# Kernel optimization log

Hardware: AMD Instinct MI355X
Metric: run time of the kernel (lower is better)

The kernel has to match this reference:

```python
import jax, jax.numpy as jnp
import numpy as np

EMBED_DIM = 768
OUT_DIM = 768
EPS = 1e-06


def setup_inputs() -> dict:
    key = jax.random.key(0)
    ks = jax.random.split(key, 7)
    s_in = 1.0 / np.sqrt(EMBED_DIM)
    x = jax.random.normal(ks[0], (32, 1024, EMBED_DIM), dtype=jnp.float32)
    Wq = jax.random.normal(ks[1], (OUT_DIM, EMBED_DIM), dtype=jnp.float32) * s_in
    bq = jax.random.normal(ks[2], (OUT_DIM,), dtype=jnp.float32) * 0.01
    Wk = jax.random.normal(ks[3], (OUT_DIM, EMBED_DIM), dtype=jnp.float32) * s_in
    bk = jax.random.normal(ks[4], (OUT_DIM,), dtype=jnp.float32) * 0.01
    Wv = jax.random.normal(ks[5], (OUT_DIM, EMBED_DIM), dtype=jnp.float32) * s_in
    bv = jax.random.normal(ks[6], (OUT_DIM,), dtype=jnp.float32) * 0.01
    return {"x": x, "Wq": Wq, "bq": bq, "Wk": Wk, "bk": bk, "Wv": Wv, "bv": bv}


def reference(x, Wq, bq, Wk, bk, Wv, bv):
    # Q/K/V projections: nn.Linear computes x @ W.T + b
    Q = jnp.einsum('bnd,od->bno', x, Wq) + bq  # [B, N, O]
    K = jnp.einsum('bnd,od->bno', x, Wk) + bk
    V = jnp.einsum('bnd,od->bno', x, Wv) + bv
    scale = jnp.sqrt(jnp.asarray(OUT_DIM, dtype=x.dtype)) + EPS
    attn = jnp.einsum('bqo,bko->bqk', Q, K) / scale  # [B, N, N]
    weights = jax.nn.softmax(attn, axis=-1)
    # dropout p=0.0 -> identity (eval/inference)
    return jnp.einsum('bqk,bko->bqo', weights, V)
```

## Files before the change

kernel.cpp:

```cpp
#include <hip/hip_runtime.h>
#include <hip/hip_bf16.h>


typedef float  floatx4  __attribute__((ext_vector_type(4)));
typedef float  floatx16 __attribute__((ext_vector_type(16)));
typedef short  short8   __attribute__((ext_vector_type(8)));

__device__ __forceinline__ unsigned cvtpk(float lo, float hi) {
    unsigned r;
    asm("v_cvt_pk_bf16_f32 %0, %1, %2" : "=v"(r) : "v"(lo), "v"(hi));
    return r;
}
__device__ __forceinline__ floatx16 mfma32(short8 a, short8 b, floatx16 c) {
    return __builtin_amdgcn_mfma_f32_32x32x16_bf16(a, b, c, 0, 0, 0);
}
__device__ __forceinline__ void load_lds16(const void* g, void* lds) {
    __builtin_amdgcn_global_load_lds(
        (const __attribute__((address_space(1))) unsigned int*)g,
        (__attribute__((address_space(3))) unsigned int*)lds, 16, 0, 0);
}
__device__ __forceinline__ void bar_lds() {
    asm volatile("s_waitcnt lgkmcnt(0)" ::: "memory");
    __builtin_amdgcn_s_barrier();
    __builtin_amdgcn_sched_barrier(0);
}
__device__ __forceinline__ void bar_vm() {
    asm volatile("s_waitcnt vmcnt(0)" ::: "memory");
    __builtin_amdgcn_s_barrier();
    __builtin_amdgcn_sched_barrier(0);
}

__global__ __launch_bounds__(256) void cvt_bf16(
    const float* __restrict__ s0, unsigned short* __restrict__ d0, int n0,
    const float* __restrict__ s1, unsigned short* __restrict__ d1, int n1,
    const float* __restrict__ s2, unsigned short* __restrict__ d2, int n2,
    const float* __restrict__ W,  unsigned short* __restrict__ Wf)
{
    if (blockIdx.x >= 2048) {
        const int i = (blockIdx.x - 2048) * 256 + threadIdx.x;
        const int o  = i / 96;
        const int d0i = (i % 96) * 8;
        const floatx4* s = (const floatx4*)(W + (size_t)o * 768 + d0i);
        floatx4 v0 = s[0], v1 = s[1];
        uint4 st;
        st.x = cvtpk(v0[0], v0[1]);
        st.y = cvtpk(v0[2], v0[3]);
        st.z = cvtpk(v1[0], v1[1]);
        st.w = cvtpk(v1[2], v1[3]);
        const size_t idx = (((size_t)(o >> 5) * 48 + (d0i >> 4)) * 64
                            + ((o & 31) | (((d0i >> 3) & 1) << 5))) * 8;
        *reinterpret_cast<uint4*>(Wf + idx) = st;
        return;
    }
    const int stride = 2048 * 256;
    const int base   = blockIdx.x * 256 + threadIdx.x;
    const float* ss[3] = {s0, s1, s2};
    unsigned short* dd[3] = {d0, d1, d2};
    const int nn[3] = {n0, n1, n2};
#pragma unroll
    for (int j = 0; j < 3; ++j) {
        const floatx4* s = (const floatx4*)ss[j];
        uint4* d = (uint4*)dd[j];
        for (int i = base; i < nn[j]; i += stride) {
            floatx4 v0 = s[2 * i];
            floatx4 v1 = s[2 * i + 1];
            uint4 o;
            o.x = cvtpk(v0[0], v0[1]);
            o.y = cvtpk(v0[2], v0[3]);
            o.z = cvtpk(v1[0], v1[1]);
            o.w = cvtpk(v1[2], v1[3]);
            d[i] = o;
        }
    }
}

template <int MODE>
__global__ __launch_bounds__(256, 2) void gemm_lds(
    const unsigned short* __restrict__ A,
    const unsigned short* __restrict__ B,
    unsigned short* __restrict__ C, const float* __restrict__ bias,
    float alpha)
{
    __shared__ __align__(16) unsigned short As[2][128 * 64];
    __shared__ __align__(16) unsigned short Bs[2][128 * 64];

    const int tid = threadIdx.x;
    const int l   = tid & 63;
    const int w   = tid >> 6;
    const int wr  = w >> 1;
    const int wc  = w & 1;
    const int lo5 = l & 31;
    const int hi  = l >> 5;
    const int i0  = blockIdx.x * 128;
    const int j0  = blockIdx.y * 128;

    const int srow = l >> 3;
    const int sc16 = (l & 7) ^ srow;
    const unsigned short* Ag = A + (size_t)(i0 + srow) * 768 + sc16 * 8;
    const unsigned short* Bg = B + (size_t)(j0 + srow) * 768 + sc16 * 8;

    floatx16 acc[2][2] = {};

    auto STAGE = [&](int buf, int kt) {
        const int k0 = kt * 64;
#pragma unroll
        for (int t4 = 0; t4 < 4; ++t4) {
            const int t = w * 4 + t4;
            load_lds16(Ag + (size_t)t * 8 * 768 + k0, &As[buf][t * 512]);
            load_lds16(Bg + (size_t)t * 8 * 768 + k0, &Bs[buf][t * 512]);
        }
    };
    auto COMPUTE = [&](int buf) {
        const char* Ab = (const char*)As[buf];
        const char* Bb = (const char*)Bs[buf];
#pragma unroll
        for (int kk = 0; kk < 4; ++kk) {
            short8 a[2], b[2];
#pragma unroll
            for (int i = 0; i < 2; ++i) {
                const int r = wr * 64 + i * 32 + lo5;
                const unsigned off = r * 128 + ((unsigned)((kk * 2 + hi) ^ (r & 7)) << 4);
                a[i] = *reinterpret_cast<const short8*>(Ab + off);
            }
#pragma unroll
            for (int j = 0; j < 2; ++j) {
                const int r = wc * 64 + j * 32 + lo5;
                const unsigned off = r * 128 + ((unsigned)((kk * 2 + hi) ^ (r & 7)) << 4);
                b[j] = *reinterpret_cast<const short8*>(Bb + off);
            }
#pragma unroll
            for (int i = 0; i < 2; ++i)
#pragma unroll
                for (int j = 0; j < 2; ++j)
                    acc[i][j] = mfma32(a[i], b[j], acc[i][j]);
        }
    };

    STAGE(0, 0);
    __syncthreads();
#pragma unroll 1
    for (int kt = 0; kt < 12; ++kt) {
        if (kt + 1 < 12) STAGE((kt + 1) & 1, kt + 1);
        COMPUTE(kt & 1);
        __syncthreads();
    }

#pragma unroll
    for (int i = 0; i < 2; ++i) {
        float bvv[16];
        if (MODE == 0) {
#pragma unroll
            for (int r = 0; r < 16; ++r) {
                const int ol = (r & 3) + 8 * (r >> 2) + 4 * hi;
                bvv[r] = bias[i0 + wr * 64 + i * 32 + ol];
            }
        }
#pragma unroll
        for (int j = 0; j < 2; ++j) {
            float bj = 0.f;
            if (MODE == 1) bj = bias[j0 + wc * 64 + j * 32 + lo5];
            float v[16];
#pragma unroll
            for (int r = 0; r < 16; ++r)
                v[r] = (MODE == 0) ? (acc[i][j][r] + bvv[r]) * alpha
                                   : (acc[i][j][r] + bj);
#pragma unroll
            for (int cc = 0; cc < 2; ++cc) {
                unsigned w0 = cvtpk(v[8 * cc + 0], v[8 * cc + 1]);
                unsigned w1 = cvtpk(v[8 * cc + 2], v[8 * cc + 3]);
                unsigned w2 = cvtpk(v[8 * cc + 4], v[8 * cc + 5]);
                unsigned w3 = cvtpk(v[8 * cc + 6], v[8 * cc + 7]);
                unsigned x0 = __shfl_xor(w0, 32);
                unsigned x1 = __shfl_xor(w1, 32);
                unsigned x2 = __shfl_xor(w2, 32);
                unsigned x3 = __shfl_xor(w3, 32);
                uint4 st;
                st.x = hi ? x2 : w0;
                st.y = hi ? x3 : w1;
                st.z = hi ? w2 : x0;
                st.w = hi ? w3 : x1;
                size_t idx;
                if (MODE == 0) {
                    const int og = i0 + wr * 64 + i * 32 + cc * 16;
                    const int mg = j0 + wc * 64 + j * 32 + lo5;
                    idx = ((size_t)(mg >> 5) * 48 + (og >> 4)) * 512
                        + (size_t)(lo5 | (hi << 5)) * 8;
                } else {
                    const int ng = i0 + wr * 64 + i * 32 + cc * 16;
                    const int dg = j0 + wc * 64 + j * 32 + lo5;
                    idx = ((size_t)(ng >> 4) * 24 + (dg >> 5)) * 512
                        + (size_t)(lo5 | (hi << 5)) * 8;
                }
                *reinterpret_cast<uint4*>(C + idx) = st;
            }
        }
    }
}

__global__ __launch_bounds__(512, 1) void attn_kernel(
    const unsigned short* __restrict__ Wqf,
    const unsigned short* __restrict__ Kf,
    const unsigned short* __restrict__ Vf,
    const float* __restrict__ x,
    const float* __restrict__ bq,
    float* __restrict__ out)
{
    __shared__ __align__(16) unsigned short Q_lds[96 * 512];
    __shared__ __align__(16) unsigned short P_lds[2][32 * 512];

    const int tid = threadIdx.x;
    const int l   = tid & 63;
    const int w   = tid >> 6;
    const int lo5 = l & 31;
    const int hi  = l >> 5;

    const int bid = blockIdx.x;
    const int xcd = bid & 7;
    const int jj  = bid >> 3;
    const int b   = (jj >> 4) * 8 + xcd;
    const int qi  = jj & 15;
    const int q0  = qi * 64;

    const float MFIX  = 12.0f;
    const float alpha = 1.0f / (sqrtf(768.0f) + 1e-6f);

    const short8* Kp = reinterpret_cast<const short8*>(Kf)
                       + ((size_t)b * 32 * 48) * 64 + l;
    const short8* Vp = reinterpret_cast<const short8*>(Vf)
                       + ((size_t)b * 64 * 24) * 64 + l;

    floatx16 acc6[6] = {};
    short8 kbuf[8], vbuf[4][3];

    {
        float* Xs0 = (float*)P_lds[0];
        float* Xs1 = (float*)P_lds[1];
        const float* xg = x + (size_t)(b * 1024 + q0) * 768;
        const short8* Wp = reinterpret_cast<const short8*>(Wqf) + l;

        const int c16 = tid & 31;
        const int r0  = tid >> 5;

        auto XSTAGE = [&](int p, float* Xs) {
#pragma unroll
            for (int it = 0; it < 4; ++it) {
                const int row = it * 16 + r0;
                const int u   = it * 512 + tid;
                load_lds16(xg + (size_t)row * 768 + p * 128 + ((c16 ^ (row & 7)) << 2),
                           &Xs[u * 4]);
            }
        };

        XSTAGE(0, Xs0);
        bar_vm();

        short8 wbuf2[2][3];
#pragma unroll 1
        for (int p = 0; p < 6; ++p) {
            float* Xs = (p & 1) ? Xs1 : Xs0;
#pragma unroll
            for (int jo = 0; jo < 3; ++jo)
                wbuf2[0][jo] = Wp[(size_t)((w * 3 + jo) * 48 + p * 8) * 64];
            if (p + 1 < 6) XSTAGE(p + 1, (p & 1) ? Xs0 : Xs1);
#pragma unroll
            for (int it = 0; it < 8; ++it) {
                const int ks = p * 8 + it;
                if (it + 1 < 8) {
#pragma unroll
                    for (int jo = 0; jo < 3; ++jo)
                        wbuf2[(it + 1) & 1][jo] =
                            Wp[(size_t)((w * 3 + jo) * 48 + ks + 1) * 64];
                }
                short8 xf[2];
#pragma unroll
                for (int jq = 0; jq < 2; ++jq) {
                    const int row = jq * 32 + lo5;
                    const int un  = it * 4 + hi * 2;
                    floatx4 f0 = *reinterpret_cast<const floatx4*>(
                        &Xs[((row << 5) + ((un + 0) ^ (row & 7))) * 4]);
                    floatx4 f1 = *reinterpret_cast<const floatx4*>(
                        &Xs[((row << 5) + ((un + 1) ^ (row & 7))) * 4]);
                    unsigned q0w = cvtpk(f0[0], f0[1]);
                    unsigned q1w = cvtpk(f0[2], f0[3]);
                    unsigned q2w = cvtpk(f1[0], f1[1]);
                    unsigned q3w = cvtpk(f1[2], f1[3]);
                    uint4 u4 = {q0w, q1w, q2w, q3w};
                    xf[jq] = __builtin_bit_cast(short8, u4);
                }
                __builtin_amdgcn_s_setprio(1);
#pragma unroll
                for (int jo = 0; jo < 3; ++jo) {
#pragma unroll
                    for (int jq = 0; jq < 2; ++jq)
                        acc6[jo * 2 + jq] = mfma32(wbuf2[it & 1][jo], xf[jq],
                                                   acc6[jo * 2 + jq]);
                }
                __builtin_amdgcn_s_setprio(0);
            }
            bar_vm();
        }

        {
            const short8* Kc0 = Kp + (size_t)w * 48 * 64;
#pragma unroll
            for (int u = 0; u < 8; ++u) kbuf[u] = Kc0[(size_t)u * 64];
        }

#pragma unroll
        for (int jo = 0; jo < 3; ++jo) {
            const int o32 = w * 96 + jo * 32;
            float bvv[16];
#pragma unroll
            for (int r = 0; r < 16; ++r)
                bvv[r] = bq[o32 + (r & 3) + 8 * (r >> 2) + 4 * hi];
#pragma unroll
            for (int jq = 0; jq < 2; ++jq) {
                float v[16];
#pragma unroll
                for (int r = 0; r < 16; ++r)
                    v[r] = (acc6[jo * 2 + jq][r] + bvv[r]) * alpha;
#pragma unroll
                for (int cc = 0; cc < 2; ++cc) {
                    unsigned w0 = cvtpk(v[8 * cc + 0], v[8 * cc + 1]);
                    unsigned w1 = cvtpk(v[8 * cc + 2], v[8 * cc + 3]);
                    unsigned w2 = cvtpk(v[8 * cc + 4], v[8 * cc + 5]);
                    unsigned w3 = cvtpk(v[8 * cc + 6], v[8 * cc + 7]);
                    unsigned x0 = __shfl_xor(w0, 32);
                    unsigned x1 = __shfl_xor(w1, 32);
                    unsigned x2 = __shfl_xor(w2, 32);
                    unsigned x3 = __shfl_xor(w3, 32);
                    uint4 st;
                    st.x = hi ? x2 : w0;
                    st.y = hi ? x3 : w1;
                    st.z = hi ? w2 : x0;
                    st.w = hi ? w3 : x1;
                    const int ks_t = w * 6 + jo * 2 + cc;
                    *reinterpret_cast<uint4*>(
                        &Q_lds[((ks_t * 2 + jq) * 64 + (lo5 | (hi << 5))) * 8]) = st;
                }
            }
        }
    }
    bar_lds();

#pragma unroll
    for (int i = 0; i < 6; ++i) acc6[i] = (floatx16){};

    float l_reg0 = 0.f, l_reg1 = 0.f;

#pragma unroll 1
    for (int c = 0; c < 4; ++c) {
        floatx16 s0 = {}, s1 = {};
        const short8* Kc = Kp + (size_t)(c * 8 + w) * 48 * 64;
        short8 qa0 = *reinterpret_cast<const short8*>(&Q_lds[(0 * 64 + l) * 8]);
        short8 qa1 = *reinterpret_cast<const short8*>(&Q_lds[(1 * 64 + l) * 8]);
#pragma unroll 1
        for (int ks8 = 0; ks8 < 6; ++ks8) {
#pragma unroll
            for (int u = 0; u < 8; ++u) {
                const int ks = ks8 * 8 + u;
                short8 ka = kbuf[u];
                if (ks + 8 < 48) kbuf[u] = Kc[(size_t)(ks + 8) * 64];
                short8 qn0, qn1;
                if (ks + 1 < 48) {
                    qn0 = *reinterpret_cast<const short8*>(&Q_lds[(((ks + 1) * 2 + 0) * 64 + l) * 8]);
                    qn1 = *reinterpret_cast<const short8*>(&Q_lds[(((ks + 1) * 2 + 1) * 64 + l) * 8]);
                }
                __builtin_amdgcn_s_setprio(1);
                s0 = mfma32(ka, qa0, s0);
                s1 = mfma32(ka, qa1, s1);
                __builtin_amdgcn_s_setprio(0);
                qa0 = qn0;
                qa1 = qn1;
            }
        }

        const short8* Vc = Vp + (size_t)(c * 16) * 24 * 64;
#pragma unroll
        for (int g = 0; g < 4; ++g)
#pragma unroll
            for (int jv = 0; jv < 3; ++jv)
                vbuf[g][jv] = Vc[((size_t)g * 24 + w * 3 + jv) * 64];

        if (c < 3) {
            const short8* Kn = Kp + (size_t)((c + 1) * 8 + w) * 48 * 64;
#pragma unroll
            for (int u = 0; u < 8; ++u) kbuf[u] = Kn[(size_t)u * 64];
        }

        float p0[16], p1[16];
        float sum0 = 0.f, sum1 = 0.f;
#pragma unroll
        for (int r = 0; r < 16; ++r) {
            p0[r] = __expf(s0[r] - MFIX); sum0 += p0[r];
            p1[r] = __expf(s1[r] - MFIX); sum1 += p1[r];
        }
        l_reg0 += sum0 + __shfl_xor(sum0, 32);
        l_reg1 += sum1 + __shfl_xor(sum1, 32);

        char* Pb = (char*)P_lds[c & 1];
#pragma unroll
        for (int cc = 0; cc < 2; ++cc) {
#pragma unroll
            for (int jt = 0; jt < 2; ++jt) {
                const float* p = jt ? p1 : p0;
                unsigned w0 = cvtpk(p[8 * cc + 0], p[8 * cc + 1]);
                unsigned w1 = cvtpk(p[8 * cc + 2], p[8 * cc + 3]);
                unsigned w2 = cvtpk(p[8 * cc + 4], p[8 * cc + 5]);
                unsigned w3 = cvtpk(p[8 * cc + 6], p[8 * cc + 7]);
                unsigned x0 = __shfl_xor(w0, 32);
                unsigned x1 = __shfl_xor(w1, 32);
                unsigned x2 = __shfl_xor(w2, 32);
                unsigned x3 = __shfl_xor(w3, 32);
                uint4 st;
                st.x = hi ? x2 : w0;
                st.y = hi ? x3 : w1;
                st.z = hi ? w2 : x0;
                st.w = hi ? w3 : x1;
                const unsigned off = (((unsigned)(w * 2 + cc) * 2 + jt) * 64 + l) * 16;
                *reinterpret_cast<uint4*>(Pb + off) = st;
            }
        }
        bar_lds();

        short8 pa0 = *reinterpret_cast<const short8*>(Pb + ((0 * 64 + l) * 16));
        short8 pa1 = *reinterpret_cast<const short8*>(Pb + ((1 * 64 + l) * 16));
#pragma unroll
        for (int g = 0; g < 16; ++g) {
            short8 pn0, pn1;
            if (g + 1 < 16) {
                pn0 = *reinterpret_cast<const short8*>(Pb + ((((g + 1) * 2 + 0) * 64 + l) * 16));
                pn1 = *reinterpret_cast<const short8*>(Pb + ((((g + 1) * 2 + 1) * 64 + l) * 16));
            }
            short8 v0 = vbuf[g & 3][0];
            short8 v1 = vbuf[g & 3][1];
            short8 v2 = vbuf[g & 3][2];
            if (g < 12) {
#pragma unroll
                for (int jv = 0; jv < 3; ++jv)
                    vbuf[g & 3][jv] = Vc[((size_t)(g + 4) * 24 + w * 3 + jv) * 64];
            }
            __builtin_amdgcn_s_setprio(1);
            acc6[0] = mfma32(pa0, v0, acc6[0]);
            acc6[3] = mfma32(pa1, v0, acc6[3]);
            acc6[1] = mfma32(pa0, v1, acc6[1]);
            acc6[4] = mfma32(pa1, v1, acc6[4]);
            acc6[2] = mfma32(pa0, v2, acc6[2]);
            acc6[5] = mfma32(pa1, v2, acc6[5]);
            __builtin_amdgcn_s_setprio(0);
            pa0 = pn0;
            pa1 = pn1;
        }
    }

    bar_lds();
    float* lred = (float*)Q_lds;
    if (hi == 0) {
        lred[(w * 2 + 0) * 32 + lo5] = l_reg0;
        lred[(w * 2 + 1) * 32 + lo5] = l_reg1;
    }
    bar_lds();
    float lt0 = 0.f, lt1 = 0.f;
#pragma unroll
    for (int wv = 0; wv < 8; ++wv) {
        lt0 += lred[(wv * 2 + 0) * 32 + lo5];
        lt1 += lred[(wv * 2 + 1) * 32 + lo5];
    }
    const float li0 = 1.0f / lt0;
    const float li1 = 1.0f / lt1;

#pragma unroll
    for (int jt = 0; jt < 2; ++jt)
#pragma unroll
        for (int r = 0; r < 16; ++r) {
            const int qr = (r & 3) + 8 * (r >> 2) + 4 * hi;
            const float linv = __shfl(jt ? li1 : li0, qr);
            const size_t grow = (size_t)(b * 1024 + q0 + jt * 32 + qr) * 768;
#pragma unroll
            for (int jv = 0; jv < 3; ++jv)
                out[grow + (w * 3 + jv) * 32 + lo5] = acc6[jt * 3 + jv][r] * linv;
        }
}

extern "C" void kernel_launch(void* const* d_in, const int* in_sizes, int n_in,
                              void* d_out, int out_size, void* d_ws, size_t ws_size,
                              hipStream_t stream) {
    const float* x  = (const float*)d_in[0];
    const float* Wq = (const float*)d_in[1];
    const float* bq = (const float*)d_in[2];
    const float* Wk = (const float*)d_in[3];
    const float* bk = (const float*)d_in[4];
    const float* Wv = (const float*)d_in[5];
    const float* bv = (const float*)d_in[6];
    float* out = (float*)d_out;

    unsigned short* Wqf = (unsigned short*)d_ws;
    unsigned short* Kf  = (unsigned short*)d_ws + 25165824u;
    unsigned short* Vf  = (unsigned short*)d_ws + 50331648u;

    unsigned short* xb  = (unsigned short*)d_out;
    unsigned short* Wkb = (unsigned short*)d_out + 25165824u;
    unsigned short* Wvb = Wkb + 589824u;

    cvt_bf16<<<2336, 256, 0, stream>>>(x, xb, 3145728,
                                       Wk, Wkb, 73728,
                                       Wv, Wvb, 73728,
                                       Wq, Wqf);

    gemm_lds<0><<<dim3(6, 256), 256, 0, stream>>>(Wkb, xb, Kf, bk, 1.0f);
    gemm_lds<1><<<dim3(256, 6), 256, 0, stream>>>(xb, Wvb, Vf, bv, 1.0f);

    attn_kernel<<<dim3(512), 512, 0, stream>>>(Wqf, Kf, Vf, x, bq, out);
}
```

Before: 306.1 us.

## Process 512-key chunks with two K tiles per wave, halving barrier rounds

The attention loop now covers 512 keys per outer iteration instead of 256. Each wave computes two 32-key score tiles, so every Q fragment read from LDS feeds four MFMAs instead of two, and the number of softmax/PV rounds and barriers is halved. The P buffer becomes a single larger buffer with a trailing barrier instead of double-buffering. K/V register prefetch depth is shortened, which may expose more global-load latency, while register pressure rises from the extra score accumulators.

```diff
diff --git a/kernel.cpp b/kernel.cpp
--- a/kernel.cpp
+++ b/kernel.cpp
@@ -206,7 +206,7 @@
     float* __restrict__ out)
 {
     __shared__ __align__(16) unsigned short Q_lds[96 * 512];
-    __shared__ __align__(16) unsigned short P_lds[2][32 * 512];
+    __shared__ __align__(16) unsigned short P_lds[64 * 512];
 
     const int tid = threadIdx.x;
     const int l   = tid & 63;
@@ -230,11 +230,11 @@
                        + ((size_t)b * 64 * 24) * 64 + l;
 
     floatx16 acc6[6] = {};
-    short8 kbuf[8], vbuf[4][3];
+    short8 kbA[4], kbB[4], vbuf[2][3];
 
     {
-        float* Xs0 = (float*)P_lds[0];
-        float* Xs1 = (float*)P_lds[1];
+        float* Xs0 = (float*)P_lds;
+        float* Xs1 = (float*)(P_lds + 16 * 512 * 2);
         const float* xg = x + (size_t)(b * 1024 + q0) * 768;
         const short8* Wp = reinterpret_cast<const short8*>(Wqf) + l;
 
@@ -300,10 +300,10 @@
             bar_vm();
         }
 
-        {
-            const short8* Kc0 = Kp + (size_t)w * 48 * 64;
-#pragma unroll
-            for (int u = 0; u < 8; ++u) kbuf[u] = Kc0[(size_t)u * 64];
+#pragma unroll
+        for (int u = 0; u < 4; ++u) {
+            kbA[u] = Kp[((size_t)(0 * 16 + w) * 48 + u) * 64];
+            kbB[u] = Kp[((size_t)(0 * 16 + 8 + w) * 48 + u) * 64];
         }
 
 #pragma unroll
@@ -347,113 +347,118 @@
     for (int i = 0; i < 6; ++i) acc6[i] = (floatx16){};
 
     float l_reg0 = 0.f, l_reg1 = 0.f;
+    char* Pb = (char*)P_lds;
 
 #pragma unroll 1
-    for (int c = 0; c < 4; ++c) {
-        floatx16 s0 = {}, s1 = {};
-        const short8* Kc = Kp + (size_t)(c * 8 + w) * 48 * 64;
-        short8 qa0 = *reinterpret_cast<const short8*>(&Q_lds[(0 * 64 + l) * 8]);
-        short8 qa1 = *reinterpret_cast<const short8*>(&Q_lds[(1 * 64 + l) * 8]);
+    for (int c = 0; c < 2; ++c) {
+        floatx16 sA0 = {}, sA1 = {}, sB0 = {}, sB1 = {};
+        const short8* KcA = Kp + (size_t)(c * 16 + w) * 48 * 64;
+        const short8* KcB = Kp + (size_t)(c * 16 + 8 + w) * 48 * 64;
 #pragma unroll 1
-        for (int ks8 = 0; ks8 < 6; ++ks8) {
-#pragma unroll
-            for (int u = 0; u < 8; ++u) {
-                const int ks = ks8 * 8 + u;
-                short8 ka = kbuf[u];
-                if (ks + 8 < 48) kbuf[u] = Kc[(size_t)(ks + 8) * 64];
-                short8 qn0, qn1;
-                if (ks + 1 < 48) {
-                    qn0 = *reinterpret_cast<const short8*>(&Q_lds[(((ks + 1) * 2 + 0) * 64 + l) * 8]);
-                    qn1 = *reinterpret_cast<const short8*>(&Q_lds[(((ks + 1) * 2 + 1) * 64 + l) * 8]);
-                }
+        for (int k4 = 0; k4 < 12; ++k4) {
+#pragma unroll
+            for (int u = 0; u < 4; ++u) {
+                const int ks = k4 * 4 + u;
+                short8 ka = kbA[u];
+                short8 kb = kbB[u];
+                if (ks + 4 < 48) {
+                    kbA[u] = KcA[(size_t)(ks + 4) * 64];
+                    kbB[u] = KcB[(size_t)(ks + 4) * 64];
+                }
+                short8 qa0 = *reinterpret_cast<const short8*>(&Q_lds[((ks * 2 + 0) * 64 + l) * 8]);
+                short8 qa1 = *reinterpret_cast<const short8*>(&Q_lds[((ks * 2 + 1) * 64 + l) * 8]);
                 __builtin_amdgcn_s_setprio(1);
-                s0 = mfma32(ka, qa0, s0);
-                s1 = mfma32(ka, qa1, s1);
+                sA0 = mfma32(ka, qa0, sA0);
+                sA1 = mfma32(ka, qa1, sA1);
+                sB0 = mfma32(kb, qa0, sB0);
+                sB1 = mfma32(kb, qa1, sB1);
                 __builtin_amdgcn_s_setprio(0);
-                qa0 = qn0;
-                qa1 = qn1;
-            }
-        }
-
-        const short8* Vc = Vp + (size_t)(c * 16) * 24 * 64;
-#pragma unroll
-        for (int g = 0; g < 4; ++g)
+            }
+        }
+
+        const short8* Vc = Vp + (size_t)(c * 32) * 24 * 64;
+#pragma unroll
+        for (int g = 0; g < 2; ++g)
 #pragma unroll
             for (int jv = 0; jv < 3; ++jv)
                 vbuf[g][jv] = Vc[((size_t)g * 24 + w * 3 + jv) * 64];
 
-        if (c < 3) {
-            const short8* Kn = Kp + (size_t)((c + 1) * 8 + w) * 48 * 64;
-#pragma unroll
-            for (int u = 0; u < 8; ++u) kbuf[u] = Kn[(size_t)u * 64];
-        }
-
-        float p0[16], p1[16];
+        float pA0[16], pA1[16], pB0[16], pB1[16];
         float sum0 = 0.f, sum1 = 0.f;
 #pragma unroll
         for (int r = 0; r < 16; ++r) {
-            p0[r] = __expf(s0[r] - MFIX); sum0 += p0[r];
-            p1[r] = __expf(s1[r] - MFIX); sum1 += p1[r];
+            pA0[r] = __expf(sA0[r] - MFIX); sum0 += pA0[r];
+            pA1[r] = __expf(sA1[r] - MFIX); sum1 += pA1[r];
+            pB0[r] = __expf(sB0[r] - MFIX); sum0 += pB0[r];
+            pB1[r] = __expf(sB1[r] - MFIX); sum1 += pB1[r];
         }
         l_reg0 += sum0 + __shfl_xor(sum0, 32);
         l_reg1 += sum1 + __shfl_xor(sum1, 32);
 
-        char* Pb = (char*)P_lds[c & 1];
-#pragma unroll
-        for (int cc = 0; cc < 2; ++cc) {
-#pragma unroll
-            for (int jt = 0; jt < 2; ++jt) {
-                const float* p = jt ? p1 : p0;
-                unsigned w0 = cvtpk(p[8 * cc + 0], p[8 * cc + 1]);
-                unsigned w1 = cvtpk(p[8 * cc + 2], p[8 * cc + 3]);
-                unsigned w2 = cvtpk(p[8 * cc + 4], p[8 * cc + 5]);
-                unsigned w3 = cvtpk(p[8 * cc + 6], p[8 * cc + 7]);
-                unsigned x0 = __shfl_xor(w0, 32);
-                unsigned x1 = __shfl_xor(w1, 32);
-                unsigned x2 = __shfl_xor(w2, 32);
-                unsigned x3 = __shfl_xor(w3, 32);
-                uint4 st;
-                st.x = hi ? x2 : w0;
-                st.y = hi ? x3 : w1;
-                st.z = hi ? w2 : x0;
-                st.w = hi ? w3 : x1;
-                const unsigned off = (((unsigned)(w * 2 + cc) * 2 + jt) * 64 + l) * 16;
-                *reinterpret_cast<uint4*>(Pb + off) = st;
+#pragma unroll
+        for (int S = 0; S < 2; ++S) {
+#pragma unroll
+            for (int cc = 0; cc < 2; ++cc) {
+#pragma unroll
+                for (int jt = 0; jt < 2; ++jt) {
+                    const float* p = S ? (jt ? pB1 : pB0) : (jt ? pA1 : pA0);
+                    unsigned w0 = cvtpk(p[8 * cc + 0], p[8 * cc + 1]);
+                    unsigned w1 = cvtpk(p[8 * cc + 2], p[8 * cc + 3]);
+                    unsigned w2 = cvtpk(p[8 * cc + 4], p[8 * cc + 5]);
+                    unsigned w3 = cvtpk(p[8 * cc + 6], p[8 * cc + 7]);
+                    unsigned x0 = __shfl_xor(w0, 32);
+                    unsigned x1 = __shfl_xor(w1, 32);
+                    unsigned x2 = __shfl_xor(w2, 32);
+                    unsigned x3 = __shfl_xor(w3, 32);
+                    uint4 st;
+                    st.x = hi ? x2 : w0;
+                    st.y = hi ? x3 : w1;
+                    st.z = hi ? w2 : x0;
+                    st.w = hi ? w3 : x1;
+                    const unsigned ku = (unsigned)((S ? 8 + w : w) * 2 + cc);
+                    const unsigned off = ((ku * 2 + jt) * 64 + l) * 16;
+                    *reinterpret_cast<uint4*>(Pb + off) = st;
+                }
+            }
+        }
+
+        if (c == 0) {
+#pragma unroll
+            for (int u = 0; u < 4; ++u) {
+                kbA[u] = Kp[((size_t)(16 + w) * 48 + u) * 64];
+                kbB[u] = Kp[((size_t)(16 + 8 + w) * 48 + u) * 64];
             }
         }
         bar_lds();
 
-        short8 pa0 = *reinterpret_cast<const short8*>(Pb + ((0 * 64 + l) * 16));
-        short8 pa1 = *reinterpret_cast<const short8*>(Pb + ((1 * 64 + l) * 16));
-#pragma unroll
-        for (int g = 0; g < 16; ++g) {
-            short8 pn0, pn1;
-            if (g + 1 < 16) {
-                pn0 = *reinterpret_cast<const short8*>(Pb + ((((g + 1) * 2 + 0) * 64 + l) * 16));
-                pn1 = *reinterpret_cast<const short8*>(Pb + ((((g + 1) * 2 + 1) * 64 + l) * 16));
-            }
-            short8 v0 = vbuf[g & 3][0];
-            short8 v1 = vbuf[g & 3][1];
-            short8 v2 = vbuf[g & 3][2];
-            if (g < 12) {
-#pragma unroll
-                for (int jv = 0; jv < 3; ++jv)
-                    vbuf[g & 3][jv] = Vc[((size_t)(g + 4) * 24 + w * 3 + jv) * 64];
-            }
-            __builtin_amdgcn_s_setprio(1);
-            acc6[0] = mfma32(pa0, v0, acc6[0]);
-            acc6[3] = mfma32(pa1, v0, acc6[3]);
-            acc6[1] = mfma32(pa0, v1, acc6[1]);
-            acc6[4] = mfma32(pa1, v1, acc6[4]);
-            acc6[2] = mfma32(pa0, v2, acc6[2]);
-            acc6[5] = mfma32(pa1, v2, acc6[5]);
-            __builtin_amdgcn_s_setprio(0);
-            pa0 = pn0;
-            pa1 = pn1;
-        }
-    }
-
-    bar_lds();
+#pragma unroll 1
+        for (int g2 = 0; g2 < 16; ++g2) {
+#pragma unroll
+            for (int h = 0; h < 2; ++h) {
+                const int g = g2 * 2 + h;
+                short8 v0 = vbuf[h][0];
+                short8 v1 = vbuf[h][1];
+                short8 v2 = vbuf[h][2];
+                if (g + 2 < 32) {
+#pragma unroll
+                    for (int jv = 0; jv < 3; ++jv)
+                        vbuf[h][jv] = Vc[((size_t)(g + 2) * 24 + w * 3 + jv) * 64];
+                }
+                short8 pa0 = *reinterpret_cast<const short8*>(Pb + (((g * 2 + 0) * 64 + l) * 16));
+                short8 pa1 = *reinterpret_cast<const short8*>(Pb + (((g * 2 + 1) * 64 + l) * 16));
+                __builtin_amdgcn_s_setprio(1);
+                acc6[0] = mfma32(pa0, v0, acc6[0]);
+                acc6[3] = mfma32(pa1, v0, acc6[3]);
+                acc6[1] = mfma32(pa0, v1, acc6[1]);
+                acc6[4] = mfma32(pa1, v1, acc6[4]);
+                acc6[2] = mfma32(pa0, v2, acc6[2]);
+                acc6[5] = mfma32(pa1, v2, acc6[5]);
+                __builtin_amdgcn_s_setprio(0);
+            }
+        }
+        bar_lds();
+    }
+
     float* lred = (float*)Q_lds;
     if (hi == 0) {
         lred[(w * 2 + 0) * 32 + lo5] = l_reg0;
```

New measurement: 321.2 us. 1.05x slower.

## Halve attention query tile to 32 rows for more blocks and occupancy

Applied to the files above, without the earlier changes.

The attention kernel now processes 32 query rows per block instead of 64, doubling the grid to 1024 blocks. LDS buffers and register accumulators are halved and launch bounds request up to 4 blocks per CU, so more waves can be resident to hide latency. In exchange, each block re-reads the full K and V tiles and the Wq slice, so global and L2 traffic per unit of work roughly doubles. MFMA reuse of each K/V fragment also drops from two query tiles to one.

```diff
diff --git a/kernel.cpp b/kernel.cpp
--- a/kernel.cpp
+++ b/kernel.cpp
@@ -197,7 +197,7 @@
     }
 }
 
-__global__ __launch_bounds__(512, 1) void attn_kernel(
+__global__ __launch_bounds__(512, 4) void attn_kernel(
     const unsigned short* __restrict__ Wqf,
     const unsigned short* __restrict__ Kf,
     const unsigned short* __restrict__ Vf,
@@ -205,8 +205,8 @@
     const float* __restrict__ bq,
     float* __restrict__ out)
 {
-    __shared__ __align__(16) unsigned short Q_lds[96 * 512];
-    __shared__ __align__(16) unsigned short P_lds[2][32 * 512];
+    __shared__ __align__(16) unsigned short Q_lds[48 * 512];
+    __shared__ __align__(16) unsigned short P_lds[2][16 * 512];
 
     const int tid = threadIdx.x;
     const int l   = tid & 63;
@@ -217,9 +217,9 @@
     const int bid = blockIdx.x;
     const int xcd = bid & 7;
     const int jj  = bid >> 3;
-    const int b   = (jj >> 4) * 8 + xcd;
-    const int qi  = jj & 15;
-    const int q0  = qi * 64;
+    const int b   = (jj >> 5) * 8 + xcd;
+    const int qi  = jj & 31;
+    const int q0  = qi * 32;
 
     const float MFIX  = 12.0f;
     const float alpha = 1.0f / (sqrtf(768.0f) + 1e-6f);
@@ -229,8 +229,8 @@
     const short8* Vp = reinterpret_cast<const short8*>(Vf)
                        + ((size_t)b * 64 * 24) * 64 + l;
 
-    floatx16 acc6[6] = {};
-    short8 kbuf[8], vbuf[4][3];
+    floatx16 acc3[3] = {};
+    short8 kbuf[4], vbuf[2][3];
 
     {
         float* Xs0 = (float*)P_lds[0];
@@ -238,14 +238,12 @@
         const float* xg = x + (size_t)(b * 1024 + q0) * 768;
         const short8* Wp = reinterpret_cast<const short8*>(Wqf) + l;
 
-        const int c16 = tid & 31;
-        const int r0  = tid >> 5;
-
         auto XSTAGE = [&](int p, float* Xs) {
 #pragma unroll
-            for (int it = 0; it < 4; ++it) {
-                const int row = it * 16 + r0;
+            for (int it = 0; it < 2; ++it) {
                 const int u   = it * 512 + tid;
+                const int row = u >> 5;
+                const int c16 = u & 31;
                 load_lds16(xg + (size_t)row * 768 + p * 128 + ((c16 ^ (row & 7)) << 2),
                            &Xs[u * 4]);
             }
@@ -271,143 +269,44 @@
                         wbuf2[(it + 1) & 1][jo] =
                             Wp[(size_t)((w * 3 + jo) * 48 + ks + 1) * 64];
                 }
-                short8 xf[2];
-#pragma unroll
-                for (int jq = 0; jq < 2; ++jq) {
-                    const int row = jq * 32 + lo5;
-                    const int un  = it * 4 + hi * 2;
-                    floatx4 f0 = *reinterpret_cast<const floatx4*>(
-                        &Xs[((row << 5) + ((un + 0) ^ (row & 7))) * 4]);
-                    floatx4 f1 = *reinterpret_cast<const floatx4*>(
-                        &Xs[((row << 5) + ((un + 1) ^ (row & 7))) * 4]);
-                    unsigned q0w = cvtpk(f0[0], f0[1]);
-                    unsigned q1w = cvtpk(f0[2], f0[3]);
-                    unsigned q2w = cvtpk(f1[0], f1[1]);
-                    unsigned q3w = cvtpk(f1[2], f1[3]);
-                    uint4 u4 = {q0w, q1w, q2w, q3w};
-                    xf[jq] = __builtin_bit_cast(short8, u4);
-                }
+                const int row = lo5;
+                const int un  = it * 4 + hi * 2;
+                floatx4 f0 = *reinterpret_cast<const floatx4*>(
+                    &Xs[((row << 5) + ((un + 0) ^ (row & 7))) * 4]);
+                floatx4 f1 = *reinterpret_cast<const floatx4*>(
+                    &Xs[((row << 5) + ((un + 1) ^ (row & 7))) * 4]);
+                uint4 u4;
+                u4.x = cvtpk(f0[0], f0[1]);
+                u4.y = cvtpk(f0[2], f0[3]);
+                u4.z = cvtpk(f1[0], f1[1]);
+                u4.w = cvtpk(f1[2], f1[3]);
+                short8 xf = __builtin_bit_cast(short8, u4);
                 __builtin_amdgcn_s_setprio(1);
 #pragma unroll
-                for (int jo = 0; jo < 3; ++jo) {
-#pragma unroll
-                    for (int jq = 0; jq < 2; ++jq)
-                        acc6[jo * 2 + jq] = mfma32(wbuf2[it & 1][jo], xf[jq],
-                                                   acc6[jo * 2 + jq]);
-                }
+                for (int jo = 0; jo < 3; ++jo)
+                    acc3[jo] = mfma32(wbuf2[it & 1][jo], xf, acc3[jo]);
                 __builtin_amdgcn_s_setprio(0);
             }
             bar_vm();
         }
 
-        {
-            const short8* Kc0 = Kp + (size_t)w * 48 * 64;
-#pragma unroll
-            for (int u = 0; u < 8; ++u) kbuf[u] = Kc0[(size_t)u * 64];
-        }
+#pragma unroll
+        for (int u = 0; u < 4; ++u)
+            kbuf[u] = Kp[((size_t)w * 48 + u) * 64];
 
 #pragma unroll
         for (int jo = 0; jo < 3; ++jo) {
             const int o32 = w * 96 + jo * 32;
-            float bvv[16];
+            float v[16];
 #pragma unroll
             for (int r = 0; r < 16; ++r)
-                bvv[r] = bq[o32 + (r & 3) + 8 * (r >> 2) + 4 * hi];
-#pragma unroll
-            for (int jq = 0; jq < 2; ++jq) {
-                float v[16];
-#pragma unroll
-                for (int r = 0; r < 16; ++r)
-                    v[r] = (acc6[jo * 2 + jq][r] + bvv[r]) * alpha;
-#pragma unroll
-                for (int cc = 0; cc < 2; ++cc) {
-                    unsigned w0 = cvtpk(v[8 * cc + 0], v[8 * cc + 1]);
-                    unsigned w1 = cvtpk(v[8 * cc + 2], v[8 * cc + 3]);
-                    unsigned w2 = cvtpk(v[8 * cc + 4], v[8 * cc + 5]);
-                    unsigned w3 = cvtpk(v[8 * cc + 6], v[8 * cc + 7]);
-                    unsigned x0 = __shfl_xor(w0, 32);
-                    unsigned x1 = __shfl_xor(w1, 32);
-                    unsigned x2 = __shfl_xor(w2, 32);
-                    unsigned x3 = __shfl_xor(w3, 32);
-                    uint4 st;
-                    st.x = hi ? x2 : w0;
-                    st.y = hi ? x3 : w1;
-                    st.z = hi ? w2 : x0;
-                    st.w = hi ? w3 : x1;
-                    const int ks_t = w * 6 + jo * 2 + cc;
-                    *reinterpret_cast<uint4*>(
-                        &Q_lds[((ks_t * 2 + jq) * 64 + (lo5 | (hi << 5))) * 8]) = st;
-                }
-            }
-        }
-    }
-    bar_lds();
-
-#pragma unroll
-    for (int i = 0; i < 6; ++i) acc6[i] = (floatx16){};
-
-    float l_reg0 = 0.f, l_reg1 = 0.f;
-
-#pragma unroll 1
-    for (int c = 0; c < 4; ++c) {
-        floatx16 s0 = {}, s1 = {};
-        const short8* Kc = Kp + (size_t)(c * 8 + w) * 48 * 64;
-        short8 qa0 = *reinterpret_cast<const short8*>(&Q_lds[(0 * 64 + l) * 8]);
-        short8 qa1 = *reinterpret_cast<const short8*>(&Q_lds[(1 * 64 + l) * 8]);
-#pragma unroll 1
-        for (int ks8 = 0; ks8 < 6; ++ks8) {
-#pragma unroll
-            for (int u = 0; u < 8; ++u) {
-                const int ks = ks8 * 8 + u;
-                short8 ka = kbuf[u];
-                if (ks + 8 < 48) kbuf[u] = Kc[(size_t)(ks + 8) * 64];
-                short8 qn0, qn1;
-                if (ks + 1 < 48) {
-                    qn0 = *reinterpret_cast<const short8*>(&Q_lds[(((ks + 1) * 2 + 0) * 64 + l) * 8]);
-                    qn1 = *reinterpret_cast<const short8*>(&Q_lds[(((ks + 1) * 2 + 1) * 64 + l) * 8]);
-                }
-                __builtin_amdgcn_s_setprio(1);
-                s0 = mfma32(ka, qa0, s0);
-                s1 = mfma32(ka, qa1, s1);
-                __builtin_amdgcn_s_setprio(0);
-                qa0 = qn0;
-                qa1 = qn1;
-            }
-        }
-
-        const short8* Vc = Vp + (size_t)(c * 16) * 24 * 64;
-#pragma unroll
-        for (int g = 0; g < 4; ++g)
-#pragma unroll
-            for (int jv = 0; jv < 3; ++jv)
-                vbuf[g][jv] = Vc[((size_t)g * 24 + w * 3 + jv) * 64];
-
-        if (c < 3) {
-            const short8* Kn = Kp + (size_t)((c + 1) * 8 + w) * 48 * 64;
-#pragma unroll
-            for (int u = 0; u < 8; ++u) kbuf[u] = Kn[(size_t)u * 64];
-        }
-
-        float p0[16], p1[16];
-        float sum0 = 0.f, sum1 = 0.f;
-#pragma unroll
-        for (int r = 0; r < 16; ++r) {
-            p0[r] = __expf(s0[r] - MFIX); sum0 += p0[r];
-            p1[r] = __expf(s1[r] - MFIX); sum1 += p1[r];
-        }
-        l_reg0 += sum0 + __shfl_xor(sum0, 32);
-        l_reg1 += sum1 + __shfl_xor(sum1, 32);
-
-        char* Pb = (char*)P_lds[c & 1];
-#pragma unroll
-        for (int cc = 0; cc < 2; ++cc) {
-#pragma unroll
-            for (int jt = 0; jt < 2; ++jt) {
-                const float* p = jt ? p1 : p0;
-                unsigned w0 = cvtpk(p[8 * cc + 0], p[8 * cc + 1]);
-                unsigned w1 = cvtpk(p[8 * cc + 2], p[8 * cc + 3]);
-                unsigned w2 = cvtpk(p[8 * cc + 4], p[8 * cc + 5]);
-                unsigned w3 = cvtpk(p[8 * cc + 6], p[8 * cc + 7]);
+                v[r] = (acc3[jo][r] + bq[o32 + (r & 3) + 8 * (r >> 2) + 4 * hi]) * alpha;
+#pragma unroll
+            for (int cc = 0; cc < 2; ++cc) {
+                unsigned w0 = cvtpk(v[8 * cc + 0], v[8 * cc + 1]);
+                unsigned w1 = cvtpk(v[8 * cc + 2], v[8 * cc + 3]);
+                unsigned w2 = cvtpk(v[8 * cc + 4], v[8 * cc + 5]);
+                unsigned w3 = cvtpk(v[8 * cc + 6], v[8 * cc + 7]);
                 unsigned x0 = __shfl_xor(w0, 32);
                 unsigned x1 = __shfl_xor(w1, 32);
                 unsigned x2 = __shfl_xor(w2, 32);
@@ -417,69 +316,120 @@
                 st.y = hi ? x3 : w1;
                 st.z = hi ? w2 : x0;
                 st.w = hi ? w3 : x1;
-                const unsigned off = (((unsigned)(w * 2 + cc) * 2 + jt) * 64 + l) * 16;
-                *reinterpret_cast<uint4*>(Pb + off) = st;
-            }
+                const int ks_t = w * 6 + jo * 2 + cc;
+                *reinterpret_cast<uint4*>(
+                    &Q_lds[((size_t)(ks_t * 64 + (lo5 | (hi << 5)))) * 8]) = st;
+            }
+        }
+    }
+    bar_lds();
+
+#pragma unroll
+    for (int i = 0; i < 3; ++i) acc3[i] = (floatx16){};
+
+    float l_reg = 0.f;
+
+#pragma unroll 1
+    for (int c = 0; c < 4; ++c) {
+        floatx16 s = {};
+        const short8* Kc = Kp + (size_t)(c * 8 + w) * 48 * 64;
+#pragma unroll 1
+        for (int k4 = 0; k4 < 12; ++k4) {
+#pragma unroll
+            for (int u = 0; u < 4; ++u) {
+                const int ks = k4 * 4 + u;
+                short8 ka = kbuf[u];
+                if (ks + 4 < 48) kbuf[u] = Kc[(size_t)(ks + 4) * 64];
+                short8 qa = *reinterpret_cast<const short8*>(
+                    &Q_lds[((size_t)(ks * 64 + l)) * 8]);
+                __builtin_amdgcn_s_setprio(1);
+                s = mfma32(ka, qa, s);
+                __builtin_amdgcn_s_setprio(0);
+            }
+        }
+
+        const short8* Vc = Vp + (size_t)(c * 16) * 24 * 64;
+#pragma unroll
+        for (int g = 0; g < 2; ++g)
+#pragma unroll
+            for (int jv = 0; jv < 3; ++jv)
+                vbuf[g][jv] = Vc[((size_t)g * 24 + w * 3 + jv) * 64];
+
+        if (c < 3) {
+            const short8* Kn = Kp + (size_t)((c + 1) * 8 + w) * 48 * 64;
+#pragma unroll
+            for (int u = 0; u < 4; ++u) kbuf[u] = Kn[(size_t)u * 64];
+        }
+
+        float sum = 0.f;
+#pragma unroll
+        for (int r = 0; r < 16; ++r) {
+            s[r] = __expf(s[r] - MFIX);
+            sum += s[r];
+        }
+        l_reg += sum + __shfl_xor(sum, 32);
+
+        char* Pb = (char*)P_lds[c & 1];
+#pragma unroll
+        for (int cc = 0; cc < 2; ++cc) {
+            unsigned w0 = cvtpk(s[8 * cc + 0], s[8 * cc + 1]);
+            unsigned w1 = cvtpk(s[8 * cc + 2], s[8 * cc + 3]);
+            unsigned w2 = cvtpk(s[8 * cc + 4], s[8 * cc + 5]);
+            unsigned w3 = cvtpk(s[8 * cc + 6], s[8 * cc + 7]);
+            unsigned x0 = __shfl_xor(w0, 32);
+            unsigned x1 = __shfl_xor(w1, 32);
+            unsigned x2 = __shfl_xor(w2, 32);
+            unsigned x3 = __shfl_xor(w3, 32);
+            uint4 st;
+            st.x = hi ? x2 : w0;
+            st.y = hi ? x3 : w1;
+            st.z = hi ? w2 : x0;
+            st.w = hi ? w3 : x1;
+            const unsigned off = (((unsigned)(w * 2 + cc)) * 64 + l) * 16;
+            *reinterpret_cast<uint4*>(Pb + off) = st;
         }
         bar_lds();
 
-        short8 pa0 = *reinterpret_cast<const short8*>(Pb + ((0 * 64 + l) * 16));
-        short8 pa1 = *reinterpret_cast<const short8*>(Pb + ((1 * 64 + l) * 16));
-#pragma unroll
-        for (int g = 0; g < 16; ++g) {
-            short8 pn0, pn1;
-            if (g + 1 < 16) {
-                pn0 = *reinterpret_cast<const short8*>(Pb + ((((g + 1) * 2 + 0) * 64 + l) * 16));
-                pn1 = *reinterpret_cast<const short8*>(Pb + ((((g + 1) * 2 + 1) * 64 + l) * 16));
-            }
-            short8 v0 = vbuf[g & 3][0];
-            short8 v1 = vbuf[g & 3][1];
-            short8 v2 = vbuf[g & 3][2];
-            if (g < 12) {
-#pragma unroll
-                for (int jv = 0; jv < 3; ++jv)
-                    vbuf[g & 3][jv] = Vc[((size_t)(g + 4) * 24 + w * 3 + jv) * 64];
-            }
-            __builtin_amdgcn_s_setprio(1);
-            acc6[0] = mfma32(pa0, v0, acc6[0]);
-            acc6[3] = mfma32(pa1, v0, acc6[3]);
-            acc6[1] = mfma32(pa0, v1, acc6[1]);
-            acc6[4] = mfma32(pa1, v1, acc6[4]);
-            acc6[2] = mfma32(pa0, v2, acc6[2]);
-            acc6[5] = mfma32(pa1, v2, acc6[5]);
-            __builtin_amdgcn_s_setprio(0);
-            pa0 = pn0;
-            pa1 = pn1;
-        }
-    }
-
+#pragma unroll 1
+        for (int g2 = 0; g2 < 8; ++g2) {
+#pragma unroll
+            for (int h = 0; h < 2; ++h) {
+                const int g = g2 * 2 + h;
+                short8 v0 = vbuf[h][0];
+                short8 v1 = vbuf[h][1];
+                short8 v2 = vbuf[h][2];
+                if (g + 2 < 16) {
+#pragma unroll
+                    for (int jv = 0; jv < 3; ++jv)
+                        vbuf[h][jv] = Vc[((size_t)(g + 2) * 24 + w * 3 + jv) * 64];
+                }
+                short8 pa = *reinterpret_cast<const short8*>(Pb + (((g * 64) + l) * 16));
+                __builtin_amdgcn_s_setprio(1);
+                acc3[0] = mfma32(pa, v0, acc3[0]);
+                acc3[1] = mfma32(pa, v1, acc3[1]);
+                acc3[2] = mfma32(pa, v2, acc3[2]);
+                __builtin_amdgcn_s_setprio(0);
+            }
+        }
+    }
+
+    float* lred = (float*)Q_lds;
+    if (hi == 0) lred[w * 32 + lo5] = l_reg;
     bar_lds();
-    float* lred = (float*)Q_lds;
-    if (hi == 0) {
-        lred[(w * 2 + 0) * 32 + lo5] = l_reg0;
-        lred[(w * 2 + 1) * 32 + lo5] = l_reg1;
-    }
-    bar_lds();
-    float lt0 = 0.f, lt1 = 0.f;
-#pragma unroll
-    for (int wv = 0; wv < 8; ++wv) {
-        lt0 += lred[(wv * 2 + 0) * 32 + lo5];
-        lt1 += lred[(wv * 2 + 1) * 32 + lo5];
-    }
-    const float li0 = 1.0f / lt0;
-    const float li1 = 1.0f / lt1;
-
-#pragma unroll
-    for (int jt = 0; jt < 2; ++jt)
-#pragma unroll
-        for (int r = 0; r < 16; ++r) {
-            const int qr = (r & 3) + 8 * (r >> 2) + 4 * hi;
-            const float linv = __shfl(jt ? li1 : li0, qr);
-            const size_t grow = (size_t)(b * 1024 + q0 + jt * 32 + qr) * 768;
-#pragma unroll
-            for (int jv = 0; jv < 3; ++jv)
-                out[grow + (w * 3 + jv) * 32 + lo5] = acc6[jt * 3 + jv][r] * linv;
-        }
+    float lt = 0.f;
+#pragma unroll
+    for (int wv = 0; wv < 8; ++wv) lt += lred[wv * 32 + lo5];
+    const float li = 1.0f / lt;
+
+#pragma unroll
+    for (int r = 0; r < 16; ++r) {
+        const int qr = (r & 3) + 8 * (r >> 2) + 4 * hi;
+        const float linv = __shfl(li, qr);
+        const size_t grow = (size_t)(b * 1024 + q0 + qr) * 768;
+#pragma unroll
+        for (int jv = 0; jv < 3; ++jv)
+            out[grow + (w * 3 + jv) * 32 + lo5] = acc3[jv][r] * linv;
+    }
 }
 
 extern "C" void kernel_launch(void* const* d_in, const int* in_sizes, int n_in,
@@ -510,5 +460,5 @@
     gemm_lds<0><<<dim3(6, 256), 256, 0, stream>>>(Wkb, xb, Kf, bk, 1.0f);
     gemm_lds<1><<<dim3(256, 6), 256, 0, stream>>>(xb, Wvb, Vf, bv, 1.0f);
 
-    attn_kernel<<<dim3(512), 512, 0, stream>>>(Wqf, Kf, Vf, x, bq, out);
-}
+    attn_kernel<<<dim3(1024), 512, 0, stream>>>(Wqf, Kf, Vf, x, bq, out);
+}
```

After: 359.3 us. +17.4%, slower.
